# Optimization experiments

Hardware: AMD Instinct MI355X
Metric: run time of the kernel (lower is better)

## Reference

```python
import jax, jax.numpy as jnp
import numpy as np

B, T, H = 256, 2048, 128

def setup_inputs() -> dict:
    key = jax.random.key(0)
    ks = jax.random.split(key, 8)
    s = 1.0 / np.sqrt(H)  # PyTorch LSTM/Linear init: U(-1/sqrt(H), 1/sqrt(H))
    u = lambda k, shape: jax.random.uniform(k, shape, jnp.float32, -s, s)
    return {
        "x": jax.random.normal(ks[0], (B, T, 1), jnp.float32),
        "W_ih": u(ks[1], (4 * H, 1)),   # gate order: i, f, g, o
        "W_hh": u(ks[2], (4 * H, H)),
        "b_ih": u(ks[3], (4 * H,)),
        "b_hh": u(ks[4], (4 * H,)),
        "fc_w": u(ks[5], (1, H)),
        "fc_b": u(ks[6], (1,)),
    }

def _lstm(x, W_ih, W_hh, b_ih, b_hh):
    Bx = x.shape[0]
    Hh = W_hh.shape[1]
    # precompute input contribution to all gates: [B, T, 4H]
    xg = jnp.einsum('bti,gi->btg', x, W_ih) + b_ih + b_hh

    def step(carry, xg_t):
        h, c = carry
        g = xg_t + h @ W_hh.T                      # [B, 4H]
        i, f, gg, o = jnp.split(g, 4, axis=-1)
        i = jax.nn.sigmoid(i)
        f = jax.nn.sigmoid(f)
        gg = jnp.tanh(gg)
        o = jax.nn.sigmoid(o)
        c = f * c + i * gg
        h = o * jnp.tanh(c)
        return (h, c), h

    h0 = jnp.zeros((Bx, Hh), x.dtype)
    (hT, cT), hs = jax.lax.scan(step, (h0, h0), jnp.swapaxes(xg, 0, 1))
    return jnp.swapaxes(hs, 0, 1), hT, cT          # [B,T,H], [B,H], [B,H]

def reference(x, W_ih, W_hh, b_ih, b_hh, fc_w, fc_b):
    hs, hT, cT = _lstm(x, W_ih, W_hh, b_ih, b_hh)
    out = jnp.tanh(hs @ fc_w.T + fc_b)             # [B, T, 1]
    # num_layers=1 -> leading layer dim of 1 on h, c (PyTorch convention)
    return out, (hT[None], cT[None])
```

## Files before the change

kernel.cpp:

```cpp
#include <hip/hip_runtime.h>


typedef _Float16 half2v __attribute__((ext_vector_type(2)));
typedef _Float16 f16x8  __attribute__((ext_vector_type(8)));
typedef float    f32x4  __attribute__((ext_vector_type(4)));

constexpr int NB = 256;
constexpr int NT = 2048;
constexpr int NH = 128;

__device__ __forceinline__ float fexp2(float x) {
    float r;
    asm("v_exp_f32 %0, %1" : "=v"(r) : "v"(x));
    return r;
}
__device__ __forceinline__ float frcp(float x) {
    float r;
    asm("v_rcp_f32 %0, %1" : "=v"(r) : "v"(x));
    return r;
}
__device__ __forceinline__ float fsig(float x) {
    return frcp(1.f + fexp2(x * -1.44269504f));
}
__device__ __forceinline__ float ftanh(float x) {
    return fmaf(2.f, frcp(1.f + fexp2(x * -2.88539008f)), -1.f);
}

__device__ __forceinline__ unsigned packh2(float lo, float hi) {
    half2v p;
    p.x = (_Float16)lo;
    p.y = (_Float16)hi;
    return __builtin_bit_cast(unsigned, p);
}

__device__ __forceinline__ float dot2(unsigned int w, unsigned int h, float acc) {
    half2v a = __builtin_bit_cast(half2v, w);
    half2v b = __builtin_bit_cast(half2v, h);
#if __has_builtin(__builtin_amdgcn_fdot2)
    return __builtin_amdgcn_fdot2(a, b, acc, false);
#else
    float r;
    asm("v_dot2_f32_f16 %0, %1, %2, %3" : "=v"(r) : "v"(a), "v"(b), "v"(acc));
    return r;
#endif
}

__device__ __forceinline__ f32x4 mfma32(f16x8 a, f16x8 b, f32x4 c) {
#if __has_builtin(__builtin_amdgcn_mfma_f32_16x16x32_f16)
    return __builtin_amdgcn_mfma_f32_16x16x32_f16(a, b, c, 0, 0, 0);
#else
    asm("v_mfma_f32_16x16x32_f16 %0, %1, %2, %0" : "+v"(c) : "v"(a), "v"(b));
    return c;
#endif
}

__device__ __forceinline__ void barrier_lds() {
    asm volatile("s_waitcnt lgkmcnt(0)" ::: "memory");
    __builtin_amdgcn_s_barrier();
    asm volatile("" ::: "memory");
}

template <bool DEFER_FC>
__global__ __launch_bounds__(512, 2)
void lstm_k1(const float* __restrict__ x, const float* __restrict__ W_ih,
             const float* __restrict__ W_hh, const float* __restrict__ b_ih,
             const float* __restrict__ b_hh, const float* __restrict__ fc_w,
             const float* __restrict__ fc_b, float* __restrict__ out,
             _Float16* __restrict__ hws) {
    __shared__ __align__(16) float    x_lds[NT];
    __shared__ __align__(16) _Float16 h_lds[2][NH];
    __shared__ float red[8];

    const int b    = blockIdx.x;
    const int t    = threadIdx.x;
    const int lane = t & 63;
    const int w    = t >> 6;
    const int q    = lane >> 4;
    const int nlo  = lane & 15;
    const int u    = 16 * w + nlo;

    ((float4*)x_lds)[t] = ((const float4*)(x + (size_t)b * NT))[t];
    if (t < NH) h_lds[0][t] = (_Float16)0.f;

    f16x8 bw[4][4];
#pragma unroll
    for (int g = 0; g < 4; ++g) {
        const float* wrow = W_hh + (size_t)(g * NH + u) * NH;
#pragma unroll
        for (int kc = 0; kc < 4; ++kc) {
            float4 f0 = *(const float4*)(wrow + kc * 32 + q * 8);
            float4 f1 = *(const float4*)(wrow + kc * 32 + q * 8 + 4);
            f16x8 v;
            v[0] = (_Float16)f0.x; v[1] = (_Float16)f0.y;
            v[2] = (_Float16)f0.z; v[3] = (_Float16)f0.w;
            v[4] = (_Float16)f1.x; v[5] = (_Float16)f1.y;
            v[6] = (_Float16)f1.z; v[7] = (_Float16)f1.w;
            bw[g][kc] = v;
        }
    }
#pragma unroll
    for (int g = 0; g < 4; ++g)
#pragma unroll
        for (int kc = 0; kc < 4; ++kc) asm volatile("" : "+v"(bw[g][kc]));

    const float bi = b_ih[u] + b_hh[u];
    const float bf = b_ih[NH + u] + b_hh[NH + u];
    const float bz = b_ih[2 * NH + u] + b_hh[2 * NH + u];
    const float bo = b_ih[3 * NH + u] + b_hh[3 * NH + u];
    const float wi = W_ih[u];
    const float wf = W_ih[NH + u];
    const float wz = W_ih[2 * NH + u];
    const float wo = W_ih[3 * NH + u];

    float c = 0.f, h = 0.f;
    float fcw = 0.f, fcb = 0.f;
    if (!DEFER_FC) {
        fcw = fc_w[u];
        fcb = fc_b[0];
    }

    float*    outp = out + (size_t)b * NT;
    _Float16* hrow = DEFER_FC ? (hws + (size_t)b * NT * NH) : (_Float16*)nullptr;

    __syncthreads();

    for (int step = 0; step < NT; ++step) {
        const _Float16* hbuf = h_lds[step & 1];
        f16x8 av[4];
#pragma unroll
        for (int kc = 0; kc < 4; ++kc)
            av[kc] = *(const f16x8*)(hbuf + kc * 32 + q * 8);

        f32x4 a0 = {0.f, 0.f, 0.f, 0.f}, a1 = a0, a2 = a0, a3 = a0;
#pragma unroll
        for (int kc = 0; kc < 4; ++kc) {
            a0 = mfma32(av[kc], bw[0][kc], a0);
            a1 = mfma32(av[kc], bw[1][kc], a1);
            a2 = mfma32(av[kc], bw[2][kc], a2);
            a3 = mfma32(av[kc], bw[3][kc], a3);
        }

        float xv = x_lds[step];
        float gi = fsig(fmaf(xv, wi, a0[0] + bi));
        float gf = fsig(fmaf(xv, wf, a1[0] + bf));
        float gz = ftanh(fmaf(xv, wz, a2[0] + bz));
        float go = fsig(fmaf(xv, wo, a3[0] + bo));

        c = fmaf(gf, c, gi * gz);
        h = go * ftanh(c);
        if (lane < 16) {
            h_lds[(step + 1) & 1][u] = (_Float16)h;
            if (DEFER_FC) hrow[(size_t)step * NH + u] = (_Float16)h;
        }
        if (!DEFER_FC) {
            float p = (lane < 16) ? h * fcw : 0.f;
#pragma unroll
            for (int m = 8; m >= 1; m >>= 1) p += __shfl_xor(p, m, 64);
            if (lane == 0) red[w] = p;
            __syncthreads();
            if (t == 0) {
                float s = red[0] + red[1] + red[2] + red[3] + red[4] + red[5] +
                          red[6] + red[7];
                outp[step] = ftanh(s + fcb);
            }
        }
        barrier_lds();
    }

    if (lane < 16) {
        float* hT = out + (size_t)NB * NT;
        float* cT = hT + (size_t)NB * NH;
        hT[b * NH + u] = h;
        cT[b * NH + u] = c;
    }
}

__global__ __launch_bounds__(256) void fc_k2(const _Float16* __restrict__ hws,
                                             const float* __restrict__ fc_w,
                                             const float* __restrict__ fc_b,
                                             float* __restrict__ out) {
    __shared__ unsigned wlds[64];
    const int t = threadIdx.x;
    if (t < 64) {
        float2 f = ((const float2*)fc_w)[t];
        wlds[t] = packh2(f.x, f.y);
    }
    __syncthreads();

    const size_t idx = (size_t)blockIdx.x * 256 + t;
    const uint4* hp = (const uint4*)(hws + idx * NH);
    const uint4* wp = (const uint4*)wlds;
    float acc = 0.f;
#pragma unroll
    for (int j = 0; j < 16; ++j) {
        uint4 hv = hp[j];
        uint4 wv = wp[j];
        acc = dot2(hv.x, wv.x, acc);
        acc = dot2(hv.y, wv.y, acc);
        acc = dot2(hv.z, wv.z, acc);
        acc = dot2(hv.w, wv.w, acc);
    }
    out[idx] = ftanh(acc + fc_b[0]);
}

extern "C" void kernel_launch(void* const* d_in, const int* in_sizes, int n_in,
                              void* d_out, int out_size, void* d_ws, size_t ws_size,
                              hipStream_t stream) {
    const float* x    = (const float*)d_in[0];
    const float* W_ih = (const float*)d_in[1];
    const float* W_hh = (const float*)d_in[2];
    const float* b_ih = (const float*)d_in[3];
    const float* b_hh = (const float*)d_in[4];
    const float* fc_w = (const float*)d_in[5];
    const float* fc_b = (const float*)d_in[6];
    float* out = (float*)d_out;

    const size_t need = (size_t)NB * NT * NH * sizeof(_Float16);
    if (ws_size >= need) {
        _Float16* hws = (_Float16*)d_ws;
        lstm_k1<true><<<dim3(NB), dim3(512), 0, stream>>>(
            x, W_ih, W_hh, b_ih, b_hh, fc_w, fc_b, out, hws);
        fc_k2<<<dim3(NB * NT / 256), dim3(256), 0, stream>>>(hws, fc_w, fc_b, out);
    } else {
        lstm_k1<false><<<dim3(NB), dim3(512), 0, stream>>>(
            x, W_ih, W_hh, b_ih, b_hh, fc_w, fc_b, out, nullptr);
    }
}
```

Baseline: 937.8 us.

## Halve waves per block, each wave computing two hidden-unit groups

Reduces the LSTM block from 8 waves to 4, so each wave computes 32 hidden units using 8 independent MFMA accumulator chains per step. The input projection and bias are folded into the MFMA accumulator's initial value. The aim is cheaper per-step barriers and more instruction-level parallelism to hide MFMA latency. In exchange, each wave does twice the MFMA and activation work on the serial critical path and holds twice as many weight registers.

```diff
diff --git a/kernel.cpp b/kernel.cpp
--- a/kernel.cpp
+++ b/kernel.cpp
@@ -61,7 +61,7 @@
 }
 
 template <bool DEFER_FC>
-__global__ __launch_bounds__(512, 2)
+__global__ __launch_bounds__(256, 1)
 void lstm_k1(const float* __restrict__ x, const float* __restrict__ W_ih,
              const float* __restrict__ W_hh, const float* __restrict__ b_ih,
              const float* __restrict__ b_hh, const float* __restrict__ fc_w,
@@ -69,7 +69,7 @@
              _Float16* __restrict__ hws) {
     __shared__ __align__(16) float    x_lds[NT];
     __shared__ __align__(16) _Float16 h_lds[2][NH];
-    __shared__ float red[8];
+    __shared__ float red[4];
 
     const int b    = blockIdx.x;
     const int t    = threadIdx.x;
@@ -77,46 +77,57 @@
     const int w    = t >> 6;
     const int q    = lane >> 4;
     const int nlo  = lane & 15;
-    const int u    = 16 * w + nlo;
-
-    ((float4*)x_lds)[t] = ((const float4*)(x + (size_t)b * NT))[t];
+    const int u0   = 32 * w + nlo;
+    const int u1   = u0 + 16;
+
+    ((float4*)x_lds)[t]       = ((const float4*)(x + (size_t)b * NT))[t];
+    ((float4*)x_lds)[t + 256] = ((const float4*)(x + (size_t)b * NT))[t + 256];
     if (t < NH) h_lds[0][t] = (_Float16)0.f;
 
-    f16x8 bw[4][4];
+    f16x8 bw[8][4];
 #pragma unroll
     for (int g = 0; g < 4; ++g) {
-        const float* wrow = W_hh + (size_t)(g * NH + u) * NH;
-#pragma unroll
-        for (int kc = 0; kc < 4; ++kc) {
-            float4 f0 = *(const float4*)(wrow + kc * 32 + q * 8);
-            float4 f1 = *(const float4*)(wrow + kc * 32 + q * 8 + 4);
-            f16x8 v;
-            v[0] = (_Float16)f0.x; v[1] = (_Float16)f0.y;
-            v[2] = (_Float16)f0.z; v[3] = (_Float16)f0.w;
-            v[4] = (_Float16)f1.x; v[5] = (_Float16)f1.y;
-            v[6] = (_Float16)f1.z; v[7] = (_Float16)f1.w;
-            bw[g][kc] = v;
-        }
-    }
-#pragma unroll
-    for (int g = 0; g < 4; ++g)
-#pragma unroll
-        for (int kc = 0; kc < 4; ++kc) asm volatile("" : "+v"(bw[g][kc]));
-
-    const float bi = b_ih[u] + b_hh[u];
-    const float bf = b_ih[NH + u] + b_hh[NH + u];
-    const float bz = b_ih[2 * NH + u] + b_hh[2 * NH + u];
-    const float bo = b_ih[3 * NH + u] + b_hh[3 * NH + u];
-    const float wi = W_ih[u];
-    const float wf = W_ih[NH + u];
-    const float wz = W_ih[2 * NH + u];
-    const float wo = W_ih[3 * NH + u];
-
-    float c = 0.f, h = 0.f;
-    float fcw = 0.f, fcb = 0.f;
+#pragma unroll
+        for (int ub = 0; ub < 2; ++ub) {
+            const float* wrow =
+                W_hh + (size_t)(g * NH + 32 * w + 16 * ub + nlo) * NH;
+#pragma unroll
+            for (int kc = 0; kc < 4; ++kc) {
+                float4 f0 = *(const float4*)(wrow + kc * 32 + q * 8);
+                float4 f1 = *(const float4*)(wrow + kc * 32 + q * 8 + 4);
+                f16x8 v;
+                v[0] = (_Float16)f0.x; v[1] = (_Float16)f0.y;
+                v[2] = (_Float16)f0.z; v[3] = (_Float16)f0.w;
+                v[4] = (_Float16)f1.x; v[5] = (_Float16)f1.y;
+                v[6] = (_Float16)f1.z; v[7] = (_Float16)f1.w;
+                bw[2 * g + ub][kc] = v;
+            }
+        }
+    }
+#pragma unroll
+    for (int r = 0; r < 8; ++r)
+#pragma unroll
+        for (int kc = 0; kc < 4; ++kc) asm volatile("" : "+v"(bw[r][kc]));
+
+    const float bi0 = b_ih[u0] + b_hh[u0];
+    const float bf0 = b_ih[NH + u0] + b_hh[NH + u0];
+    const float bz0 = b_ih[2 * NH + u0] + b_hh[2 * NH + u0];
+    const float bo0 = b_ih[3 * NH + u0] + b_hh[3 * NH + u0];
+    const float bi1 = b_ih[u1] + b_hh[u1];
+    const float bf1 = b_ih[NH + u1] + b_hh[NH + u1];
+    const float bz1 = b_ih[2 * NH + u1] + b_hh[2 * NH + u1];
+    const float bo1 = b_ih[3 * NH + u1] + b_hh[3 * NH + u1];
+    const float wi0 = W_ih[u0], wf0 = W_ih[NH + u0];
+    const float wz0 = W_ih[2 * NH + u0], wo0 = W_ih[3 * NH + u0];
+    const float wi1 = W_ih[u1], wf1 = W_ih[NH + u1];
+    const float wz1 = W_ih[2 * NH + u1], wo1 = W_ih[3 * NH + u1];
+
+    float c0 = 0.f, h0 = 0.f, c1 = 0.f, h1 = 0.f;
+    float fcw0 = 0.f, fcw1 = 0.f, fcb = 0.f;
     if (!DEFER_FC) {
-        fcw = fc_w[u];
-        fcb = fc_b[0];
+        fcw0 = fc_w[u0];
+        fcw1 = fc_w[u1];
+        fcb  = fc_b[0];
     }
 
     float*    outp = out + (size_t)b * NT;
@@ -130,39 +141,55 @@
 #pragma unroll
         for (int kc = 0; kc < 4; ++kc)
             av[kc] = *(const f16x8*)(hbuf + kc * 32 + q * 8);
-
-        f32x4 a0 = {0.f, 0.f, 0.f, 0.f}, a1 = a0, a2 = a0, a3 = a0;
+        float xv = x_lds[step];
+
+        f32x4 ai0 = {fmaf(xv, wi0, bi0), 0.f, 0.f, 0.f};
+        f32x4 af0 = {fmaf(xv, wf0, bf0), 0.f, 0.f, 0.f};
+        f32x4 az0 = {fmaf(xv, wz0, bz0), 0.f, 0.f, 0.f};
+        f32x4 ao0 = {fmaf(xv, wo0, bo0), 0.f, 0.f, 0.f};
+        f32x4 ai1 = {fmaf(xv, wi1, bi1), 0.f, 0.f, 0.f};
+        f32x4 af1 = {fmaf(xv, wf1, bf1), 0.f, 0.f, 0.f};
+        f32x4 az1 = {fmaf(xv, wz1, bz1), 0.f, 0.f, 0.f};
+        f32x4 ao1 = {fmaf(xv, wo1, bo1), 0.f, 0.f, 0.f};
+
 #pragma unroll
         for (int kc = 0; kc < 4; ++kc) {
-            a0 = mfma32(av[kc], bw[0][kc], a0);
-            a1 = mfma32(av[kc], bw[1][kc], a1);
-            a2 = mfma32(av[kc], bw[2][kc], a2);
-            a3 = mfma32(av[kc], bw[3][kc], a3);
-        }
-
-        float xv = x_lds[step];
-        float gi = fsig(fmaf(xv, wi, a0[0] + bi));
-        float gf = fsig(fmaf(xv, wf, a1[0] + bf));
-        float gz = ftanh(fmaf(xv, wz, a2[0] + bz));
-        float go = fsig(fmaf(xv, wo, a3[0] + bo));
-
-        c = fmaf(gf, c, gi * gz);
-        h = go * ftanh(c);
+            ai0 = mfma32(av[kc], bw[0][kc], ai0);
+            ai1 = mfma32(av[kc], bw[1][kc], ai1);
+            af0 = mfma32(av[kc], bw[2][kc], af0);
+            af1 = mfma32(av[kc], bw[3][kc], af1);
+            az0 = mfma32(av[kc], bw[4][kc], az0);
+            az1 = mfma32(av[kc], bw[5][kc], az1);
+            ao0 = mfma32(av[kc], bw[6][kc], ao0);
+            ao1 = mfma32(av[kc], bw[7][kc], ao1);
+        }
+
+        float gi0 = fsig(ai0[0]), gf0 = fsig(af0[0]);
+        float gz0 = ftanh(az0[0]), go0 = fsig(ao0[0]);
+        c0 = fmaf(gf0, c0, gi0 * gz0);
+        h0 = go0 * ftanh(c0);
+        float gi1 = fsig(ai1[0]), gf1 = fsig(af1[0]);
+        float gz1 = ftanh(az1[0]), go1 = fsig(ao1[0]);
+        c1 = fmaf(gf1, c1, gi1 * gz1);
+        h1 = go1 * ftanh(c1);
+
         if (lane < 16) {
-            h_lds[(step + 1) & 1][u] = (_Float16)h;
-            if (DEFER_FC) hrow[(size_t)step * NH + u] = (_Float16)h;
+            _Float16* hnxt = h_lds[(step + 1) & 1];
+            hnxt[u0] = (_Float16)h0;
+            hnxt[u1] = (_Float16)h1;
+            if (DEFER_FC) {
+                hrow[(size_t)step * NH + u0] = (_Float16)h0;
+                hrow[(size_t)step * NH + u1] = (_Float16)h1;
+            }
         }
         if (!DEFER_FC) {
-            float p = (lane < 16) ? h * fcw : 0.f;
-#pragma unroll
-            for (int m = 8; m >= 1; m >>= 1) p += __shfl_xor(p, m, 64);
+            float p = (lane < 16) ? fmaf(h0, fcw0, h1 * fcw1) : 0.f;
+#pragma unroll
+            for (int m = 32; m >= 1; m >>= 1) p += __shfl_xor(p, m, 64);
             if (lane == 0) red[w] = p;
             __syncthreads();
-            if (t == 0) {
-                float s = red[0] + red[1] + red[2] + red[3] + red[4] + red[5] +
-                          red[6] + red[7];
-                outp[step] = ftanh(s + fcb);
-            }
+            if (t == 0)
+                outp[step] = ftanh(red[0] + red[1] + red[2] + red[3] + fcb);
         }
         barrier_lds();
     }
@@ -170,8 +197,10 @@
     if (lane < 16) {
         float* hT = out + (size_t)NB * NT;
         float* cT = hT + (size_t)NB * NH;
-        hT[b * NH + u] = h;
-        cT[b * NH + u] = c;
+        hT[b * NH + u0] = h0;
+        hT[b * NH + u1] = h1;
+        cT[b * NH + u0] = c0;
+        cT[b * NH + u1] = c1;
     }
 }
 
@@ -218,11 +247,11 @@
     const size_t need = (size_t)NB * NT * NH * sizeof(_Float16);
     if (ws_size >= need) {
         _Float16* hws = (_Float16*)d_ws;
-        lstm_k1<true><<<dim3(NB), dim3(512), 0, stream>>>(
+        lstm_k1<true><<<dim3(NB), dim3(256), 0, stream>>>(
             x, W_ih, W_hh, b_ih, b_hh, fc_w, fc_b, out, hws);
         fc_k2<<<dim3(NB * NT / 256), dim3(256), 0, stream>>>(hws, fc_w, fc_b, out);
     } else {
-        lstm_k1<false><<<dim3(NB), dim3(512), 0, stream>>>(
+        lstm_k1<false><<<dim3(NB), dim3(256), 0, stream>>>(
             x, W_ih, W_hh, b_ih, b_hh, fc_w, fc_b, out, nullptr);
     }
 }
```

New measurement: 1.146 ms. 1.22x slower.
